# Performance work log

Hardware: AMD Instinct MI355X
Metric: run time of the kernel (lower is better)

## Reference

```python
import jax, jax.numpy as jnp
import numpy as np

NEG = -1e9  # stands in for -inf in masked_fill; identical softmax output, grad-safe


def _sfu(inputs, fusion, Wr, Wg):
    # SFU: m = [x, f, x*f, x-f]; o = relu(m@Wr)*g + (1-g)*x, g = sigmoid(m@Wg)
    m = jnp.concatenate([inputs, fusion, inputs * fusion, inputs - fusion], axis=-1)
    x = jax.nn.relu(m @ Wr)
    g = jax.nn.sigmoid(m @ Wg)
    return x * g + (1.0 - g) * inputs


def _stage(U, V, cmask, qmask, E, B, p):
    # One Aligner stage = InterAlign followed by SelfAlign. Batch-first layout (b, len, d).
    Wu, bu, Wv, bv, Wri, Wgi, gi, W1, b1, W2, b2, Wrs, Wgs, gs = p
    # ---- InterAlign ----
    Ct = jax.nn.relu(U @ Wu + bu)              # (b, c, d)
    Qt = jax.nn.relu(V @ Wv + bv)              # (b, q, d)
    E0 = jnp.einsum('bcd,bqd->bcq', Ct, Qt)    # (b, c, q)
    if E is not None:
        Es = jax.nn.softmax(jnp.where(cmask[:, :, None] == 0, NEG, E), axis=1)   # softmax over c
        Bs = jax.nn.softmax(jnp.where(cmask[:, None, :] == 0, NEG, B), axis=2)   # softmax over c (cols)
        E = E0 + gi * jnp.einsum('bce,beq->bcq', Bs, Es)
    else:
        E = E0
    Ett = jax.nn.softmax(jnp.where(qmask[:, None, :] == 0, NEG, E), axis=2)
    qctx = jnp.einsum('bcq,bqd->bcd', Ett, V)  # attend question
    h = _sfu(U, qctx, Wri, Wgi)
    # ---- SelfAlign ----
    H1 = jax.nn.relu(h @ W1 + b1)
    H2 = jax.nn.relu(h @ W2 + b2)
    B0 = jnp.einsum('bcd,bed->bce', H1, H2)    # (b, c, c)
    if B is not None:
        B1s = jax.nn.softmax(jnp.where(cmask[:, :, None] == 0, NEG, B), axis=1)
        B2s = jax.nn.softmax(jnp.where(cmask[:, None, :] == 0, NEG, B), axis=2)
        B = B0 + gs * jnp.einsum('bce,bef->bcf', B2s, B1s)
    else:
        B = B0
    c = U.shape[1]
    B = B * (1.0 - jnp.eye(c, dtype=B.dtype))[None]  # masked_fill_(eye, 0.0): zero diagonal
    Btt = jax.nn.softmax(jnp.where(cmask[:, None, :] == 0, NEG, B), axis=2)
    hctx = jnp.einsum('bce,bed->bcd', Btt, h)
    Z = _sfu(h, hctx, Wrs, Wgs)
    return Z, E, B


def setup_inputs() -> dict:
    key = jax.random.key(0)
    b, c_len, q_len, d = 8, 768, 96, 768
    T = 2  # number of aligner stages
    ks = jax.random.split(key, 16)
    s = 0.02
    inp = {
        'U': jax.random.normal(ks[0], (b, c_len, d), jnp.float32),
        'V': jax.random.normal(ks[1], (b, q_len, d), jnp.float32),
        'U_mask': jax.random.randint(ks[2], (b, c_len), 0, 2).astype(jnp.int32),
        'V_mask': jax.random.randint(ks[3], (b, q_len), 0, 2).astype(jnp.int32),
        'Wu': jax.random.normal(ks[4], (T, d, d), jnp.float32) * s,
        'bu': jnp.zeros((T, d), jnp.float32),
        'Wv': jax.random.normal(ks[5], (T, d, d), jnp.float32) * s,
        'bv': jnp.zeros((T, d), jnp.float32),
        'Wr_i': jax.random.normal(ks[6], (T, 4 * d, d), jnp.float32) * s,
        'Wg_i': jax.random.normal(ks[7], (T, 4 * d, d), jnp.float32) * s,
        'gamma_i': jnp.full((T,), 3.0, jnp.float32),
        'W1': jax.random.normal(ks[8], (T, d, d), jnp.float32) * s,
        'b1': jnp.zeros((T, d), jnp.float32),
        'W2': jax.random.normal(ks[9], (T, d, d), jnp.float32) * s,
        'b2': jnp.zeros((T, d), jnp.float32),
        'Wr_s': jax.random.normal(ks[10], (T, 4 * d, d), jnp.float32) * s,
        'Wg_s': jax.random.normal(ks[11], (T, 4 * d, d), jnp.float32) * s,
        'gamma_s': jnp.full((T,), 3.0, jnp.float32),
    }
    return inp


def reference(U, V, U_mask, V_mask, Wu, bu, Wv, bv, Wr_i, Wg_i, gamma_i,
              W1, b1, W2, b2, Wr_s, Wg_s, gamma_s):
    E = None
    B = None
    x = U
    for t in range(Wu.shape[0]):  # fixed small stage loop (align_1 -> align_2)
        p = (Wu[t], bu[t], Wv[t], bv[t], Wr_i[t], Wg_i[t], gamma_i[t],
             W1[t], b1[t], W2[t], b2[t], Wr_s[t], Wg_s[t], gamma_s[t])
        x, E, B = _stage(x, V, U_mask, V_mask, E, B, p)
    return x
```

## Files before the change

kernel.cpp:

```cpp
#include <hip/hip_runtime.h>
#include <math.h>

#define NEGV -1e9f

typedef short bf16x8 __attribute__((ext_vector_type(8)));
typedef float f32x4 __attribute__((ext_vector_type(4)));
typedef unsigned short ushort8v __attribute__((ext_vector_type(8)));

static __device__ __forceinline__ unsigned short f2bf(float f) {
  unsigned int u = __float_as_uint(f);
  unsigned int r = (u + 0x7fffu + ((u >> 16) & 1u)) >> 16;
  return (unsigned short)r;
}

static __device__ __forceinline__ int xcd_swz(int lin, int nwg) {
  int q = nwg >> 3, r = nwg & 7;
  int x = lin & 7, i = lin >> 3;
  return (x < r) ? x * (q + 1) + i : r * (q + 1) + (x - r) * q + i;
}

__device__ __forceinline__ float wred_max(float v) {
  #pragma unroll
  for (int o = 32; o > 0; o >>= 1) v = fmaxf(v, __shfl_down(v, o, 64));
  return v;
}
__device__ __forceinline__ float wred_sum(float v) {
  #pragma unroll
  for (int o = 32; o > 0; o >>= 1) v += __shfl_down(v, o, 64);
  return v;
}

__global__ __launch_bounds__(256)
void softmax_row_mask(const float* __restrict__ X, const int* __restrict__ mask,
                      float* __restrict__ Y, unsigned short* __restrict__ Ybf,
                      int R, int Cn)
{
  int bz = blockIdx.y, r = blockIdx.x, tid = threadIdx.x;
  const float* xr = X + ((size_t)bz * R + r) * Cn;
  const int*   mr = mask + (size_t)bz * Cn;
  float*       yr = Y ? (Y + ((size_t)bz * R + r) * Cn) : nullptr;
  unsigned short* yb = Ybf ? (Ybf + ((size_t)bz * R + r) * Cn) : nullptr;
  __shared__ float sred[4];

  float mx = -INFINITY;
  for (int i = tid; i < Cn; i += 256) {
    float v = (mr[i] != 0) ? xr[i] : NEGV;
    mx = fmaxf(mx, v);
  }
  float wm = wred_max(mx);
  if ((tid & 63) == 0) sred[tid >> 6] = wm;
  __syncthreads();
  mx = fmaxf(fmaxf(sred[0], sred[1]), fmaxf(sred[2], sred[3]));
  __syncthreads();

  float s = 0.f;
  for (int i = tid; i < Cn; i += 256) {
    float v = (mr[i] != 0) ? xr[i] : NEGV;
    s += expf(v - mx);
  }
  float wsv = wred_sum(s);
  if ((tid & 63) == 0) sred[tid >> 6] = wsv;
  __syncthreads();
  s = sred[0] + sred[1] + sred[2] + sred[3];
  float inv = 1.0f / s;

  for (int i = tid; i < Cn; i += 256) {
    float v = (mr[i] != 0) ? xr[i] : NEGV;
    float o = expf(v - mx) * inv;
    if (yr) yr[i] = o;
    if (yb) yb[i] = f2bf(o);
  }
}

__global__ __launch_bounds__(256)
void colsm_stats(const float* __restrict__ X, const int* __restrict__ mask,
                 float* __restrict__ SM, float* __restrict__ SS, int n)
{
  int bz = blockIdx.z;
  const float* Xb = X + (size_t)bz * n * n;
  const int*   mr = mask + (size_t)bz * n;
  __shared__ float T[64][65];
  __shared__ float rm[4][64], rs[4][64];
  int j0 = blockIdx.x * 64, i0 = blockIdx.y * 64;
  int t = threadIdx.x;
  int tr = t >> 4, tc4 = (t & 15) * 4;
  int jj = t & 63, qq = t >> 6;

  #pragma unroll
  for (int r = 0; r < 4; ++r) {
    int i = tr + r * 16;
    float4 v = *reinterpret_cast<const float4*>(Xb + (size_t)(i0 + i) * n + j0 + tc4);
    int mk = mr[i0 + i];
    T[i][tc4 + 0] = mk ? v.x : NEGV;
    T[i][tc4 + 1] = mk ? v.y : NEGV;
    T[i][tc4 + 2] = mk ? v.z : NEGV;
    T[i][tc4 + 3] = mk ? v.w : NEGV;
  }
  __syncthreads();
  float m = -INFINITY, s = 0.f;
  #pragma unroll
  for (int r = 0; r < 16; ++r) {
    float v = T[qq * 16 + r][jj];
    float nm = fmaxf(m, v);
    s = s * expf(m - nm) + expf(v - nm);
    m = nm;
  }
  rm[qq][jj] = m; rs[qq][jj] = s;
  __syncthreads();
  if (t < 64) {
    float m0 = rm[0][t], m1 = rm[1][t], m2 = rm[2][t], m3 = rm[3][t];
    float fm = fmaxf(fmaxf(m0, m1), fmaxf(m2, m3));
    float fs = rs[0][t] * expf(m0 - fm) + rs[1][t] * expf(m1 - fm)
             + rs[2][t] * expf(m2 - fm) + rs[3][t] * expf(m3 - fm);
    size_t base = (((size_t)bz * gridDim.x + blockIdx.x) * gridDim.y + blockIdx.y) * 64 + t;
    SM[base] = fm; SS[base] = fs;
  }
}

__global__ __launch_bounds__(256)
void colsm_emit(const float* __restrict__ X, const int* __restrict__ mask,
                const float* __restrict__ SM, const float* __restrict__ SS,
                unsigned short* __restrict__ Y, int n)
{
  int bz = blockIdx.z;
  const float* Xb = X + (size_t)bz * n * n;
  const int*   mr = mask + (size_t)bz * n;
  unsigned short* Yb = Y + (size_t)bz * n * n;
  __shared__ float T[64][65];
  __shared__ float sm[64], sinv[64];
  int j0 = blockIdx.x * 64, i0 = blockIdx.y * 64;
  int t = threadIdx.x;
  int tr = t >> 4, tc4 = (t & 15) * 4;
  int nt = gridDim.y;

  if (t < 64) {
    size_t base = (((size_t)bz * gridDim.x + blockIdx.x) * nt) * 64 + t;
    float fm = -INFINITY;
    for (int it = 0; it < nt; ++it) fm = fmaxf(fm, SM[base + (size_t)it * 64]);
    float fs = 0.f;
    for (int it = 0; it < nt; ++it)
      fs += SS[base + (size_t)it * 64] * expf(SM[base + (size_t)it * 64] - fm);
    sm[t] = fm; sinv[t] = 1.0f / fs;
  }
  #pragma unroll
  for (int r = 0; r < 4; ++r) {
    int i = tr + r * 16;
    float4 v = *reinterpret_cast<const float4*>(Xb + (size_t)(i0 + i) * n + j0 + tc4);
    int mk = mr[i0 + i];
    T[i][tc4 + 0] = mk ? v.x : NEGV;
    T[i][tc4 + 1] = mk ? v.y : NEGV;
    T[i][tc4 + 2] = mk ? v.z : NEGV;
    T[i][tc4 + 3] = mk ? v.w : NEGV;
  }
  __syncthreads();
  #pragma unroll
  for (int r = 0; r < 4; ++r) {
    int jr = tr + r * 16;
    float fm = sm[jr], inv = sinv[jr];
    ushort4 o;
    o.x = f2bf(expf(T[tc4 + 0][jr] - fm) * inv);
    o.y = f2bf(expf(T[tc4 + 1][jr] - fm) * inv);
    o.z = f2bf(expf(T[tc4 + 2][jr] - fm) * inv);
    o.w = f2bf(expf(T[tc4 + 3][jr] - fm) * inv);
    *reinterpret_cast<ushort4*>(Yb + (size_t)(j0 + jr) * n + i0 + tc4) = o;
  }
}

__global__ __launch_bounds__(256)
void transp_f32(const float* __restrict__ X, float* __restrict__ Y,
                int R, int C, long sX, long sY)
{
  int bz = blockIdx.z;
  X += (size_t)bz * sX;
  Y += (size_t)bz * sY;
  __shared__ float T[64][65];
  int c0 = blockIdx.x * 64, r0 = blockIdx.y * 64;
  int t = threadIdx.x;
  int tr = t >> 4, tc4 = (t & 15) * 4;
  #pragma unroll
  for (int rr = 0; rr < 4; ++rr) {
    int r = tr + rr * 16;
    float4 v = make_float4(0.f, 0.f, 0.f, 0.f);
    if (c0 + tc4 < C)
      v = *reinterpret_cast<const float4*>(X + (size_t)(r0 + r) * C + c0 + tc4);
    T[r][tc4 + 0] = v.x; T[r][tc4 + 1] = v.y;
    T[r][tc4 + 2] = v.z; T[r][tc4 + 3] = v.w;
  }
  __syncthreads();
  #pragma unroll
  for (int rr = 0; rr < 4; ++rr) {
    int cc = tr + rr * 16;
    int gc = c0 + cc;
    if (gc < C) {
      float4 o = make_float4(T[tc4 + 0][cc], T[tc4 + 1][cc], T[tc4 + 2][cc], T[tc4 + 3][cc]);
      *reinterpret_cast<float4*>(Y + (size_t)gc * R + r0 + tc4) = o;
    }
  }
}

__global__ __launch_bounds__(256)
void transpV(const float* __restrict__ V, unsigned short* __restrict__ VT)
{
  int bz = blockIdx.z;
  const float* Vb = V + (size_t)bz * 96 * 768;
  unsigned short* Yb = VT + (size_t)bz * 768 * 96;
  __shared__ float T[64][65];
  int c0 = blockIdx.x * 64, r0 = blockIdx.y * 64;
  int t = threadIdx.x;
  int tr = t >> 4, tc4 = (t & 15) * 4;
  #pragma unroll
  for (int rr = 0; rr < 4; ++rr) {
    int r = tr + rr * 16;
    int gr = r0 + r;
    float4 v = make_float4(0.f, 0.f, 0.f, 0.f);
    if (gr < 96)
      v = *reinterpret_cast<const float4*>(Vb + (size_t)gr * 768 + c0 + tc4);
    T[r][tc4 + 0] = v.x; T[r][tc4 + 1] = v.y;
    T[r][tc4 + 2] = v.z; T[r][tc4 + 3] = v.w;
  }
  __syncthreads();
  #pragma unroll
  for (int rr = 0; rr < 4; ++rr) {
    int cc = tr + rr * 16;
    int gc = c0 + cc;
    #pragma unroll
    for (int e = 0; e < 4; ++e) {
      int gr = r0 + tc4 + e;
      if (gr < 96) Yb[(size_t)gc * 96 + gr] = f2bf(T[tc4 + e][cc]);
    }
  }
}

__global__ __launch_bounds__(256)
void transp_cast4(const float* __restrict__ W0, const float* __restrict__ W1a,
                  const float* __restrict__ W2a, const float* __restrict__ W3a,
                  unsigned short* __restrict__ Wt)
{
  int z = blockIdx.z;
  const float* W = (z == 0) ? W0 : (z == 1) ? W1a : (z == 2) ? W2a : W3a;
  unsigned short* Y = Wt + (size_t)z * 768 * 768;
  __shared__ float T[64][65];
  int n0 = blockIdx.x * 64, k0 = blockIdx.y * 64;
  int t = threadIdx.x;
  int tr = t >> 4, tc4 = (t & 15) * 4;
  #pragma unroll
  for (int r = 0; r < 4; ++r) {
    int k = tr + r * 16;
    float4 v = *reinterpret_cast<const float4*>(W + (size_t)(k0 + k) * 768 + n0 + tc4);
    T[k][tc4 + 0] = v.x; T[k][tc4 + 1] = v.y; T[k][tc4 + 2] = v.z; T[k][tc4 + 3] = v.w;
  }
  __syncthreads();
  #pragma unroll
  for (int r = 0; r < 4; ++r) {
    int n = tr + r * 16;
    ushort4 o;
    o.x = f2bf(T[tc4 + 0][n]); o.y = f2bf(T[tc4 + 1][n]);
    o.z = f2bf(T[tc4 + 2][n]); o.w = f2bf(T[tc4 + 3][n]);
    *reinterpret_cast<ushort4*>(Y + (size_t)(n0 + n) * 768 + k0 + tc4) = o;
  }
}

__global__ __launch_bounds__(256)
void transp_cast2(const float* __restrict__ Wa, const float* __restrict__ Wb,
                  unsigned short* __restrict__ Wt)
{
  const float* W = blockIdx.z ? Wb : Wa;
  unsigned short* Y = Wt + (size_t)blockIdx.z * 768 * 2304;
  __shared__ float T[64][65];
  int n0 = blockIdx.x * 64, k0 = blockIdx.y * 64;
  int t = threadIdx.x;
  int tr = t >> 4, tc4 = (t & 15) * 4;
  #pragma unroll
  for (int r = 0; r < 4; ++r) {
    int k = tr + r * 16;
    int gk = k0 + k;
    float4 v = *reinterpret_cast<const float4*>(W + (size_t)gk * 768 + n0 + tc4);
    if (gk < 768) {
      float4 u = *reinterpret_cast<const float4*>(W + (size_t)(gk + 2304) * 768 + n0 + tc4);
      v.x += u.x; v.y += u.y; v.z += u.z; v.w += u.w;
    } else if (gk < 1536) {
      float4 u = *reinterpret_cast<const float4*>(W + (size_t)(gk + 1536) * 768 + n0 + tc4);
      v.x -= u.x; v.y -= u.y; v.z -= u.z; v.w -= u.w;
    }
    T[k][tc4 + 0] = v.x; T[k][tc4 + 1] = v.y; T[k][tc4 + 2] = v.z; T[k][tc4 + 3] = v.w;
  }
  __syncthreads();
  #pragma unroll
  for (int r = 0; r < 4; ++r) {
    int n = tr + r * 16;
    ushort4 o;
    o.x = f2bf(T[tc4 + 0][n]); o.y = f2bf(T[tc4 + 1][n]);
    o.z = f2bf(T[tc4 + 2][n]); o.w = f2bf(T[tc4 + 3][n]);
    *reinterpret_cast<ushort4*>(Y + (size_t)(n0 + n) * 2304 + k0 + tc4) = o;
  }
}

__global__ __launch_bounds__(256)
void transp_cast(const float* __restrict__ W, unsigned short* __restrict__ Wt,
                 int K, long sW, long sWt)
{
  int bz = blockIdx.z;
  W  += (size_t)bz * sW;
  Wt += (size_t)bz * sWt;
  __shared__ float T[64][65];
  int n0 = blockIdx.x * 64, k0 = blockIdx.y * 64;
  int t = threadIdx.x;
  int tr = t >> 4, tc4 = (t & 15) * 4;
  #pragma unroll
  for (int r = 0; r < 4; ++r) {
    int k = tr + r * 16;
    float4 v = *reinterpret_cast<const float4*>(W + (size_t)(k0 + k) * 768 + n0 + tc4);
    T[k][tc4 + 0] = v.x; T[k][tc4 + 1] = v.y; T[k][tc4 + 2] = v.z; T[k][tc4 + 3] = v.w;
  }
  __syncthreads();
  #pragma unroll
  for (int r = 0; r < 4; ++r) {
    int n = tr + r * 16;
    ushort4 o;
    o.x = f2bf(T[tc4 + 0][n]); o.y = f2bf(T[tc4 + 1][n]);
    o.z = f2bf(T[tc4 + 2][n]); o.w = f2bf(T[tc4 + 3][n]);
    *reinterpret_cast<ushort4*>(Wt + (size_t)(n0 + n) * K + k0 + tc4) = o;
  }
}

__global__ __launch_bounds__(256)
void cast_bf16(const float* __restrict__ X, unsigned short* __restrict__ Y, int n8)
{
  int idx = blockIdx.x * 256 + threadIdx.x;
  if (idx >= n8) return;
  float4 a0 = *reinterpret_cast<const float4*>(X + (size_t)idx * 8);
  float4 a1 = *reinterpret_cast<const float4*>(X + (size_t)idx * 8 + 4);
  ushort8v o;
  o[0] = f2bf(a0.x); o[1] = f2bf(a0.y); o[2] = f2bf(a0.z); o[3] = f2bf(a0.w);
  o[4] = f2bf(a1.x); o[5] = f2bf(a1.y); o[6] = f2bf(a1.z); o[7] = f2bf(a1.w);
  *reinterpret_cast<ushort8v*>(Y + (size_t)idx * 8) = o;
}


template<int NB, int WAVES>
__global__ __launch_bounds__(64 * WAVES)
void mfma_gemm(const unsigned short* __restrict__ A,
               const unsigned short* __restrict__ Bt0,
               const unsigned short* __restrict__ Bt1,
               const float* __restrict__ bias0, const float* __restrict__ bias1,
               const float* __restrict__ alphap, const float* __restrict__ C0,
               float* __restrict__ F0, float* __restrict__ F1,
               unsigned short* __restrict__ O0, unsigned short* __restrict__ O1,
               int M, int N, int K,
               long sA, long sB, long sC0, long sC,
               int relu, int zerodiag,
               const float* __restrict__ Xc, unsigned short* __restrict__ McO)
{
  const int RG = WAVES / 4;
  const int TM = RG * 48;
  __shared__ unsigned short As[2][TM * 32];
  __shared__ unsigned short Bs0[2][2048];
  __shared__ unsigned short Bs1[2][NB == 2 ? 2048 : 16];

  int nx = gridDim.x, ny = gridDim.y;
  int nwg = nx * ny * gridDim.z;
  int lin = blockIdx.x + nx * (blockIdx.y + ny * blockIdx.z);
  int sw = xcd_swz(lin, nwg);
  int bxi = sw % nx; int rest = sw / nx;
  int byi = rest % ny; int bz = rest / ny;

  A   += (size_t)bz * sA;
  Bt0 += (size_t)bz * sB;
  if (NB == 2) Bt1 += (size_t)bz * sB;
  const float* C0b = C0 ? (C0 + (size_t)bz * sC0) : nullptr;

  int tid = threadIdx.x;
  int w = tid >> 6, l = tid & 63;
  int m0 = byi * TM, n0 = bxi * 64;
  int wr = w >> 2, wc = w & 3;

  int g8 = (((l & 3) ^ ((l >> 3) & 3))) * 8;
  int rowA = w * 16 + (l >> 2); if (rowA > TM - 1) rowA = TM - 1;
  int rB = n0 + (w & 3) * 16 + (l >> 2); if (rB > N - 1) rB = N - 1;
  const unsigned short* srcA  = A + (size_t)(m0 + rowA) * K + g8;
  const unsigned short* srcB0 = Bt0 + (size_t)rB * K + g8;
  const unsigned short* srcB1 = (NB == 2) ? Bt1 + (size_t)rB * K + g8 : nullptr;

#define GG_STAGE(kt, bi) do { int kk0 = (kt) * 32;                                                                        \
    if (w < TM / 16)                                                                                                      \
      __builtin_amdgcn_global_load_lds((const unsigned int*)(srcA + kk0),  (unsigned int*)&As[bi][0]  + w * 256, 16, 0, 0); \
    if (w < 4)                                                                                                            \
      __builtin_amdgcn_global_load_lds((const unsigned int*)(srcB0 + kk0), (unsigned int*)&Bs0[bi][0] + w * 256, 16, 0, 0); \
    if (NB == 2 && w >= 4)                                                                                                \
      __builtin_amdgcn_global_load_lds((const unsigned int*)(srcB1 + kk0), (unsigned int*)&Bs1[bi][0] + (w - 4) * 256, 16, 0, 0); \
  } while (0)

  f32x4 a0[3] = {};
  f32x4 a1v[3] = {};

  const int NT = K / 32;
  int prm = ((l >> 4) ^ ((l >> 1) & 3)) * 8;
  GG_STAGE(0, 0);
  __syncthreads();
  int cur = 0;
  for (int kt = 0; kt < NT; ++kt) {
    if (kt + 1 < NT) GG_STAGE(kt + 1, cur ^ 1);

    bf16x8 af[3];
    #pragma unroll
    for (int i = 0; i < 3; ++i) {
      int off = (wr * 48 + i * 16 + (l & 15)) * 32 + prm;
      af[i] = *reinterpret_cast<const bf16x8*>(&As[cur][off]);
    }
    int offB = (wc * 16 + (l & 15)) * 32 + prm;
    bf16x8 b0 = *reinterpret_cast<const bf16x8*>(&Bs0[cur][offB]);
    #pragma unroll
    for (int i = 0; i < 3; ++i)
      a0[i] = __builtin_amdgcn_mfma_f32_16x16x32_bf16(af[i], b0, a0[i], 0, 0, 0);
    if (NB == 2) {
      bf16x8 b1 = *reinterpret_cast<const bf16x8*>(&Bs1[cur][offB]);
      #pragma unroll
      for (int i = 0; i < 3; ++i)
        a1v[i] = __builtin_amdgcn_mfma_f32_16x16x32_bf16(af[i], b1, a1v[i], 0, 0, 0);
    }
    __syncthreads();
    cur ^= 1;
  }
#undef GG_STAGE

  float alpha = alphap ? alphap[0] : 1.0f;
  float* F0b = F0 ? F0 + (size_t)bz * sC : nullptr;
  float* F1b = F1 ? F1 + (size_t)bz * sC : nullptr;
  unsigned short* O0b = O0 ? O0 + (size_t)bz * sC : nullptr;
  unsigned short* O1b = O1 ? O1 + (size_t)bz * sC : nullptr;
  const float* Xcb = Xc ? Xc + (size_t)bz * 589824 : nullptr;
  unsigned short* Mcb = McO ? McO + (size_t)bz * 1769472 : nullptr;

  #pragma unroll
  for (int i = 0; i < 3; ++i) {
    #pragma unroll
    for (int qq = 0; qq < 4; ++qq) {
      int gm = m0 + wr * 48 + i * 16 + (l >> 4) * 4 + qq;
      int gn = n0 + wc * 16 + (l & 15);
      if (gn >= N) continue;
      size_t oidx = (size_t)gm * N + gn;
      float v = alpha * a0[i][qq];
      if (bias0) v += bias0[gn];
      if (relu) v = fmaxf(v, 0.f);
      if (C0b) v += C0b[oidx];
      if (zerodiag && gm == gn) v = 0.f;
      if (Mcb) {
        float xv = Xcb[(size_t)gm * 768 + gn];
        size_t mrow = (size_t)gm * 2304 + gn;
        Mcb[mrow]        = f2bf(xv);
        Mcb[mrow + 768]  = f2bf(v);
        Mcb[mrow + 1536] = f2bf(xv * v);
      }
      if (F0b) F0b[oidx] = v;
      if (O0b) O0b[oidx] = f2bf(v);
      if (NB == 2) {
        float v1 = alpha * a1v[i][qq];
        if (bias1) v1 += bias1[gn];
        if (relu) v1 = fmaxf(v1, 0.f);
        if (F1b) F1b[oidx] = v1;
        if (O1b) O1b[oidx] = f2bf(v1);
      }
    }
  }
}

__global__ __launch_bounds__(512)
void mfma_dual2(const unsigned short* __restrict__ A1,
                const unsigned short* __restrict__ B1t,
                const unsigned short* __restrict__ A2,
                const unsigned short* __restrict__ B2t,
                const float* __restrict__ alphap, float* __restrict__ F0,
                int M, int N, int K,
                long sA1, long sB1, long sA2, long sB2, long sC,
                int zerodiag)
{
  __shared__ unsigned short As1[2][3072], Bs1[2][2048];
  __shared__ unsigned short As2[2][3072], Bs2[2][2048];

  int nx = gridDim.x, ny = gridDim.y;
  int nwg = nx * ny * gridDim.z;
  int lin = blockIdx.x + nx * (blockIdx.y + ny * blockIdx.z);
  int sw = xcd_swz(lin, nwg);
  int bxi = sw % nx; int rest = sw / nx;
  int byi = rest % ny; int bz = rest / ny;

  A1  += (size_t)bz * sA1;
  B1t += (size_t)bz * sB1;
  A2  += (size_t)bz * sA2;
  B2t += (size_t)bz * sB2;

  int tid = threadIdx.x;
  int w = tid >> 6, l = tid & 63;
  int m0 = byi * 96, n0 = bxi * 64;
  int wr = w >> 2, wc = w & 3;

  int g8 = (((l & 3) ^ ((l >> 3) & 3))) * 8;
  int rowA = w * 16 + (l >> 2); if (rowA > 95) rowA = 95;
  int rB = n0 + (w & 3) * 16 + (l >> 2);
  const unsigned short* srcA1 = A1 + (size_t)(m0 + rowA) * K + g8;
  const unsigned short* srcA2 = A2 + (size_t)(m0 + rowA) * K + g8;
  const unsigned short* srcB1 = B1t + (size_t)rB * K + g8;
  const unsigned short* srcB2 = B2t + (size_t)rB * K + g8;

#define D2_STAGE(kt, bi) do { int kk0 = (kt) * 32;                                                                        \
    if (w < 6) {                                                                                                          \
      __builtin_amdgcn_global_load_lds((const unsigned int*)(srcA1 + kk0), (unsigned int*)&As1[bi][0] + w * 256, 16, 0, 0); \
      __builtin_amdgcn_global_load_lds((const unsigned int*)(srcA2 + kk0), (unsigned int*)&As2[bi][0] + w * 256, 16, 0, 0); \
    }                                                                                                                     \
    if (w < 4)                                                                                                            \
      __builtin_amdgcn_global_load_lds((const unsigned int*)(srcB1 + kk0), (unsigned int*)&Bs1[bi][0] + w * 256, 16, 0, 0); \
    else                                                                                                                  \
      __builtin_amdgcn_global_load_lds((const unsigned int*)(srcB2 + kk0), (unsigned int*)&Bs2[bi][0] + (w - 4) * 256, 16, 0, 0); \
  } while (0)

  f32x4 ac1[3] = {};
  f32x4 ac2[3] = {};

  const int NT = K / 32;
  int prm = ((l >> 4) ^ ((l >> 1) & 3)) * 8;
  D2_STAGE(0, 0);
  __syncthreads();
  int cur = 0;
  for (int kt = 0; kt < NT; ++kt) {
    if (kt + 1 < NT) D2_STAGE(kt + 1, cur ^ 1);

    int offB = (wc * 16 + (l & 15)) * 32 + prm;
    bf16x8 af1[3], af2[3];
    #pragma unroll
    for (int i = 0; i < 3; ++i) {
      int off = (wr * 48 + i * 16 + (l & 15)) * 32 + prm;
      af1[i] = *reinterpret_cast<const bf16x8*>(&As1[cur][off]);
      af2[i] = *reinterpret_cast<const bf16x8*>(&As2[cur][off]);
    }
    bf16x8 b1 = *reinterpret_cast<const bf16x8*>(&Bs1[cur][offB]);
    bf16x8 b2 = *reinterpret_cast<const bf16x8*>(&Bs2[cur][offB]);
    #pragma unroll
    for (int i = 0; i < 3; ++i) {
      ac1[i] = __builtin_amdgcn_mfma_f32_16x16x32_bf16(af1[i], b1, ac1[i], 0, 0, 0);
      ac2[i] = __builtin_amdgcn_mfma_f32_16x16x32_bf16(af2[i], b2, ac2[i], 0, 0, 0);
    }
    __syncthreads();
    cur ^= 1;
  }
#undef D2_STAGE

  float alpha = alphap[0];
  float* F0b = F0 + (size_t)bz * sC;
  #pragma unroll
  for (int i = 0; i < 3; ++i) {
    #pragma unroll
    for (int qq = 0; qq < 4; ++qq) {
      int gm = m0 + wr * 48 + i * 16 + (l >> 4) * 4 + qq;
      int gn = n0 + wc * 16 + (l & 15);
      float v = ac1[i][qq] + alpha * ac2[i][qq];
      if (zerodiag && gm == gn) v = 0.f;
      F0b[(size_t)gm * N + gn] = v;
    }
  }
}

__global__ __launch_bounds__(512)
void sfu_mfma(const unsigned short* __restrict__ Mc,
              const unsigned short* __restrict__ Brt,
              const unsigned short* __restrict__ Bgt,
              const float* __restrict__ Xres, float* __restrict__ Z,
              unsigned short* __restrict__ Zb)
{
  __shared__ unsigned short As[2][3072];
  __shared__ unsigned short Brs[2][2048];
  __shared__ unsigned short Bgs[2][2048];
  const int K = 2304;
  const int NT = 72;

  int nx = gridDim.x, ny = gridDim.y;
  int nwg = nx * ny;
  int lin = blockIdx.x + nx * blockIdx.y;
  int sw = xcd_swz(lin, nwg);
  int bxi = sw % nx; int byi = sw / nx;

  int tid = threadIdx.x;
  int w = tid >> 6, l = tid & 63;
  int m0 = byi * 96, n0 = bxi * 64;
  int wr = w >> 2, wc = w & 3;

  int g8 = (((l & 3) ^ ((l >> 3) & 3))) * 8;
  int rowA = w * 16 + (l >> 2); if (rowA > 95) rowA = 95;
  int rB = n0 + (w & 3) * 16 + (l >> 2);
  const unsigned short* srcA = Mc  + (size_t)(m0 + rowA) * K + g8;
  const unsigned short* srcR = Brt + (size_t)rB * K + g8;
  const unsigned short* srcG = Bgt + (size_t)rB * K + g8;

#define SFU_STAGE(kt, bi) do { int kk0 = (kt) * 32;                                                                      \
    if (w < 6)                                                                                                           \
      __builtin_amdgcn_global_load_lds((const unsigned int*)(srcA + kk0), (unsigned int*)&As[bi][0]  + w * 256, 16, 0, 0); \
    if (w < 4)                                                                                                           \
      __builtin_amdgcn_global_load_lds((const unsigned int*)(srcR + kk0), (unsigned int*)&Brs[bi][0] + w * 256, 16, 0, 0); \
    if (w >= 4)                                                                                                          \
      __builtin_amdgcn_global_load_lds((const unsigned int*)(srcG + kk0), (unsigned int*)&Bgs[bi][0] + (w - 4) * 256, 16, 0, 0); \
  } while (0)

  f32x4 aR[3] = {};
  f32x4 aG[3] = {};

  int prm = ((l >> 4) ^ ((l >> 1) & 3)) * 8;
  SFU_STAGE(0, 0);
  __syncthreads();
  int cur = 0;
  for (int kt = 0; kt < NT; ++kt) {
    if (kt + 1 < NT) SFU_STAGE(kt + 1, cur ^ 1);

    bf16x8 af[3];
    #pragma unroll
    for (int i = 0; i < 3; ++i) {
      int off = (wr * 48 + i * 16 + (l & 15)) * 32 + prm;
      af[i] = *reinterpret_cast<const bf16x8*>(&As[cur][off]);
    }
    int offB = (wc * 16 + (l & 15)) * 32 + prm;
    bf16x8 br = *reinterpret_cast<const bf16x8*>(&Brs[cur][offB]);
    bf16x8 bg = *reinterpret_cast<const bf16x8*>(&Bgs[cur][offB]);
    #pragma unroll
    for (int i = 0; i < 3; ++i) {
      aR[i] = __builtin_amdgcn_mfma_f32_16x16x32_bf16(af[i], br, aR[i], 0, 0, 0);
      aG[i] = __builtin_amdgcn_mfma_f32_16x16x32_bf16(af[i], bg, aG[i], 0, 0, 0);
    }
    __syncthreads();
    cur ^= 1;
  }
#undef SFU_STAGE

  #pragma unroll
  for (int i = 0; i < 3; ++i) {
    #pragma unroll
    for (int qq = 0; qq < 4; ++qq) {
      int gm = m0 + wr * 48 + i * 16 + (l >> 4) * 4 + qq;
      int gn = n0 + wc * 16 + (l & 15);
      float r = fmaxf(aR[i][qq], 0.f);
      float g = 1.0f / (1.0f + expf(-aG[i][qq]));
      float xv = Xres[(size_t)gm * 768 + gn];
      float z = r * g + (1.0f - g) * xv;
      Z[(size_t)gm * 768 + gn] = z;
      if (Zb) Zb[(size_t)gm * 768 + gn] = f2bf(z);
    }
  }
}

static void launch_mfma1(const unsigned short* A, const unsigned short* Bt,
                         const float* bias, const float* alphap, const float* C0,
                         float* F0, unsigned short* O0,
                         int M, int N, int K, long sA, long sB, long sC0, long sC,
                         int relu, int zd, int batch, int tm, hipStream_t s,
                         const float* xcat = nullptr, unsigned short* mco = nullptr)
{
  dim3 g((N + 63) / 64, M / tm, batch);
  if (tm == 48)
    mfma_gemm<1, 4><<<g, 256, 0, s>>>(A, Bt, nullptr, bias, nullptr, alphap, C0,
                                      F0, nullptr, O0, nullptr, M, N, K, sA, sB, sC0, sC, relu, zd,
                                      xcat, mco);
  else
    mfma_gemm<1, 8><<<g, 512, 0, s>>>(A, Bt, nullptr, bias, nullptr, alphap, C0,
                                      F0, nullptr, O0, nullptr, M, N, K, sA, sB, sC0, sC, relu, zd,
                                      xcat, mco);
}

static void launch_mfma2(const unsigned short* A, const unsigned short* Bt0,
                         const unsigned short* Bt1, const float* bias0, const float* bias1,
                         unsigned short* O0, unsigned short* O1,
                         int M, int N, int K, long sA, long sB,
                         int relu, int batch, hipStream_t s)
{
  dim3 g((N + 63) / 64, M / 96, batch);
  mfma_gemm<2, 8><<<g, 512, 0, s>>>(A, Bt0, Bt1, bias0, bias1, nullptr, nullptr,
                                    nullptr, nullptr, O0, O1, M, N, K, sA, sB, 0, sA,
                                    relu, 0, nullptr, nullptr);
}

static void launch_sfu_tail(const float* Wr, const float* Wg, const float* xres,
                            float* z, unsigned short* zb,
                            unsigned short* Mc, unsigned short* Wt, hipStream_t s)
{
  unsigned short* Wrt = Wt;
  unsigned short* Wgt = Wt + (size_t)768 * 2304;
  transp_cast2<<<dim3(12, 36, 2), 256, 0, s>>>(Wr, Wg, Wt);
  sfu_mfma<<<dim3(12, 64), 512, 0, s>>>(Mc, Wrt, Wgt, xres, z, zb);
}

extern "C" void kernel_launch(void* const* d_in, const int* in_sizes, int n_in,
                              void* d_out, int out_size, void* d_ws, size_t ws_size,
                              hipStream_t stream)
{
  const int b = 8, c = 768, q = 96, d = 768, T = 2;
  const float* U   = (const float*)d_in[0];
  const float* V   = (const float*)d_in[1];
  const int*   Um  = (const int*)d_in[2];
  const int*   Vm  = (const int*)d_in[3];
  const float* Wu  = (const float*)d_in[4];
  const float* bu  = (const float*)d_in[5];
  const float* Wv  = (const float*)d_in[6];
  const float* bv  = (const float*)d_in[7];
  const float* Wri = (const float*)d_in[8];
  const float* Wgi = (const float*)d_in[9];
  const float* gi  = (const float*)d_in[10];
  const float* W1  = (const float*)d_in[11];
  const float* b1  = (const float*)d_in[12];
  const float* W2  = (const float*)d_in[13];
  const float* b2  = (const float*)d_in[14];
  const float* Wrs = (const float*)d_in[15];
  const float* Wgs = (const float*)d_in[16];
  const float* gs  = (const float*)d_in[17];
  float* out = (float*)d_out;

  const size_t big = (size_t)b * c * d;
  const size_t smE = (size_t)b * c * q;
  float* ws   = (float*)d_ws;
  float* xbuf = ws + 0 * big;
  float* h    = ws + 1 * big;
  float* Bm   = ws + 2 * big;
  float* t1   = ws + 3 * big;
  float* t2   = ws + 4 * big;
  float* t3   = ws + 5 * big;
  float* t4   = ws + 6 * big;
  float* Ebuf = ws + 7 * big;
  float* E0b  = Ebuf + smE;
  float* Esb  = E0b + smE;
  float* spare = Esb + smE;
  float* slotE = spare + smE;
  float* WTf  = slotE + big / 2;

  unsigned short* Mc  = (unsigned short*)t1;
  unsigned short* Wt  = (unsigned short*)t4;
  unsigned short* t1h = (unsigned short*)t1;
  unsigned short* t3h = (unsigned short*)t3;
  unsigned short* t3h2 = t3h + big;
  unsigned short* slotEb = (unsigned short*)slotE;
  unsigned short* H1b = t1h;
  unsigned short* H2b = H1b + big;
  float* SMst = spare;
  float* SSst = spare + 73728;
  unsigned short* WuT = (unsigned short*)WTf;
  unsigned short* WvT  = WuT  + (size_t)d * d;
  unsigned short* W1T  = WvT  + (size_t)d * d;
  unsigned short* W2T  = W1T  + (size_t)d * d;
  unsigned short* Vb16 = W2T  + (size_t)d * d;
  unsigned short* Qtbb = Vb16 + smE;
  unsigned short* VTb  = Qtbb + smE;
  unsigned short* EsTb = VTb  + smE;
  unsigned short* Ettb = EsTb + smE;

  const long cd = (long)c * d, cq = (long)c * q, qd = (long)q * d, cc = (long)c * c;
  const size_t dd = (size_t)d * d;
  const int cast_big = (int)(big / 8);
  (void)ws_size;

  const float* x = U;
  for (int t = 0; t < T; ++t) {
    const float* Writ = Wri + (size_t)t * 4 * dd;
    const float* Wgit = Wgi + (size_t)t * 4 * dd;
    const float* Wrst = Wrs + (size_t)t * 4 * dd;
    const float* Wgst = Wgs + (size_t)t * 4 * dd;

    transp_cast4<<<dim3(12, 12, 4), 256, 0, stream>>>(Wu + t * dd, Wv + t * dd,
                                                      W1 + t * dd, W2 + t * dd, WuT);
    if (t == 0) {
      cast_bf16<<<dim3((int)(smE / 8 / 256)), 256, 0, stream>>>(V, Vb16, (int)(smE / 8));
      transpV<<<dim3(12, 2, b), 256, 0, stream>>>(V, VTb);
      cast_bf16<<<dim3(cast_big / 256), 256, 0, stream>>>(x, t3h, cast_big);
    }

    launch_mfma1(t3h, WuT, bu + t * d, nullptr, nullptr, nullptr, t1h,
                 b * c, d, d, 0, 0, 0, 0, 1, 0, 1, 96, stream);
    launch_mfma1(Vb16, WvT, bv + t * d, nullptr, nullptr, nullptr, Qtbb,
                 b * q, d, d, 0, 0, 0, 0, 1, 0, 1, 48, stream);
    float* e0dst = (t == 0) ? Ebuf : E0b;
    launch_mfma1(t1h, Qtbb, nullptr, nullptr, nullptr, e0dst, nullptr,
                 c, q, d, cd, qd, 0, cq, 0, 0, b, 48, stream);
    if (t > 0) {
      transp_f32<<<dim3(2, 12, b), 256, 0, stream>>>(Ebuf, Esb, c, q, cq, cq);
      softmax_row_mask<<<dim3(q, b), 256, 0, stream>>>(Esb, Um, nullptr, EsTb, q, c);
      softmax_row_mask<<<dim3(c, b), 256, 0, stream>>>(Bm, Um, nullptr, slotEb, c, c);
      launch_mfma1(slotEb, EsTb, nullptr, gi + t, E0b, Ebuf, nullptr,
                   c, q, c, cc, cq, cq, cq, 0, 0, b, 48, stream);
    }
    softmax_row_mask<<<dim3(c, b), 256, 0, stream>>>(Ebuf, Vm, nullptr, Ettb, c, q);
    launch_mfma1(Ettb, VTb, nullptr, nullptr, nullptr, nullptr, nullptr,
                 c, d, q, cq, qd, 0, cd, 0, 0, b, 96, stream, x, Mc);
    launch_sfu_tail(Writ, Wgit, x, h, t3h, Mc, Wt, stream);
    launch_mfma2(t3h, W1T, W2T, b1 + t * d, b2 + t * d, H1b, H2b,
                 b * c, d, d, 0, 0, 1, 1, stream);
    if (t == 0) {
      launch_mfma1(H1b, H2b, nullptr, nullptr, nullptr, Bm, nullptr,
                   c, c, d, cd, cd, 0, cc, 0, 1, b, 96, stream);
    } else {
      colsm_stats<<<dim3(12, 12, b), 256, 0, stream>>>(Bm, Um, SMst, SSst, c);
      colsm_emit<<<dim3(12, 12, b), 256, 0, stream>>>(Bm, Um, SMst, SSst, t3h2, c);
      mfma_dual2<<<dim3(12, 8, b), 512, 0, stream>>>(H1b, H2b, slotEb, t3h2,
                                                     gs + t, Bm,
                                                     c, c, d, cd, cd, cc, cc, cc, 1);
    }
    softmax_row_mask<<<dim3(c, b), 256, 0, stream>>>(Bm, Um, nullptr, t3h2, c, c);
    transp_cast<<<dim3(12, 12, b), 256, 0, stream>>>(h, slotEb, 768, cd, cd);
    launch_mfma1(t3h2, slotEb, nullptr, nullptr, nullptr, nullptr, nullptr,
                 c, d, c, cc, cd, 0, cd, 0, 0, b, 96, stream, h, Mc);
    float* zdst = (t == T - 1) ? out : xbuf;
    unsigned short* zb16 = (t == T - 1) ? nullptr : t3h;
    launch_sfu_tail(Wrst, Wgst, h, zdst, zb16, Mc, Wt, stream);

    x = xbuf;
  }
}
```

Baseline: 714.1 us.

## Fuse Ct/Qt projections, fuse question softmax into qctx GEMM, transpose bf16 h

Result: faster. 669.3 us (-6.3%).

```diff
diff --git a/kernel.cpp b/kernel.cpp
--- a/kernel.cpp
+++ b/kernel.cpp
@@ -199,6 +199,34 @@
 }
 
 __global__ __launch_bounds__(256)
+void transp_bf16(const unsigned short* __restrict__ X, unsigned short* __restrict__ Y)
+{
+  int bz = blockIdx.z;
+  X += (size_t)bz * 589824;
+  Y += (size_t)bz * 589824;
+  __shared__ unsigned short T[64][65];
+  int c0 = blockIdx.x * 64, r0 = blockIdx.y * 64;
+  int t = threadIdx.x;
+  int tr = t >> 4, tc4 = (t & 15) * 4;
+  #pragma unroll
+  for (int rr = 0; rr < 4; ++rr) {
+    int r = tr + rr * 16;
+    ushort4 v = *reinterpret_cast<const ushort4*>(X + (size_t)(r0 + r) * 768 + c0 + tc4);
+    T[r][tc4 + 0] = v.x; T[r][tc4 + 1] = v.y;
+    T[r][tc4 + 2] = v.z; T[r][tc4 + 3] = v.w;
+  }
+  __syncthreads();
+  #pragma unroll
+  for (int rr = 0; rr < 4; ++rr) {
+    int cc = tr + rr * 16;
+    ushort4 o;
+    o.x = T[tc4 + 0][cc]; o.y = T[tc4 + 1][cc];
+    o.z = T[tc4 + 2][cc]; o.w = T[tc4 + 3][cc];
+    *reinterpret_cast<ushort4*>(Y + (size_t)(c0 + cc) * 768 + r0 + tc4) = o;
+  }
+}
+
+__global__ __launch_bounds__(256)
 void transpV(const float* __restrict__ V, unsigned short* __restrict__ VT)
 {
   int bz = blockIdx.z;
@@ -292,34 +320,6 @@
     o.x = f2bf(T[tc4 + 0][n]); o.y = f2bf(T[tc4 + 1][n]);
     o.z = f2bf(T[tc4 + 2][n]); o.w = f2bf(T[tc4 + 3][n]);
     *reinterpret_cast<ushort4*>(Y + (size_t)(n0 + n) * 2304 + k0 + tc4) = o;
-  }
-}
-
-__global__ __launch_bounds__(256)
-void transp_cast(const float* __restrict__ W, unsigned short* __restrict__ Wt,
-                 int K, long sW, long sWt)
-{
-  int bz = blockIdx.z;
-  W  += (size_t)bz * sW;
-  Wt += (size_t)bz * sWt;
-  __shared__ float T[64][65];
-  int n0 = blockIdx.x * 64, k0 = blockIdx.y * 64;
-  int t = threadIdx.x;
-  int tr = t >> 4, tc4 = (t & 15) * 4;
-  #pragma unroll
-  for (int r = 0; r < 4; ++r) {
-    int k = tr + r * 16;
-    float4 v = *reinterpret_cast<const float4*>(W + (size_t)(k0 + k) * 768 + n0 + tc4);
-    T[k][tc4 + 0] = v.x; T[k][tc4 + 1] = v.y; T[k][tc4 + 2] = v.z; T[k][tc4 + 3] = v.w;
-  }
-  __syncthreads();
-  #pragma unroll
-  for (int r = 0; r < 4; ++r) {
-    int n = tr + r * 16;
-    ushort4 o;
-    o.x = f2bf(T[tc4 + 0][n]); o.y = f2bf(T[tc4 + 1][n]);
-    o.z = f2bf(T[tc4 + 2][n]); o.w = f2bf(T[tc4 + 3][n]);
-    *reinterpret_cast<ushort4*>(Wt + (size_t)(n0 + n) * K + k0 + tc4) = o;
   }
 }
 
@@ -465,6 +465,190 @@
 }
 
 __global__ __launch_bounds__(512)
+void mfma_relu_pair(const unsigned short* __restrict__ A1g,
+                    const unsigned short* __restrict__ B1g,
+                    const float* __restrict__ bias1g, unsigned short* __restrict__ O1g,
+                    const unsigned short* __restrict__ A2g,
+                    const unsigned short* __restrict__ B2g,
+                    const float* __restrict__ bias2g, unsigned short* __restrict__ O2g)
+{
+  const int K = 768, N = 768, NT = 24;
+  __shared__ unsigned short As[2][3072];
+  __shared__ unsigned short Bs0[2][2048];
+
+  int nx = gridDim.x, ny = gridDim.y;
+  int nwg = nx * ny;
+  int lin = blockIdx.x + nx * blockIdx.y;
+  int sw = xcd_swz(lin, nwg);
+  int bxi = sw % nx; int byi = sw / nx;
+
+  const unsigned short* A; const unsigned short* Bt;
+  const float* bias; unsigned short* O;
+  int m0;
+  if (byi < 64) { A = A1g; Bt = B1g; bias = bias1g; O = O1g; m0 = byi * 96; }
+  else          { A = A2g; Bt = B2g; bias = bias2g; O = O2g; m0 = (byi - 64) * 96; }
+
+  int tid = threadIdx.x;
+  int w = tid >> 6, l = tid & 63;
+  int n0 = bxi * 64;
+  int wr = w >> 2, wc = w & 3;
+
+  int g8 = (((l & 3) ^ ((l >> 3) & 3))) * 8;
+  int rowA = w * 16 + (l >> 2); if (rowA > 95) rowA = 95;
+  int rB = n0 + (w & 3) * 16 + (l >> 2);
+  const unsigned short* srcA  = A + (size_t)(m0 + rowA) * K + g8;
+  const unsigned short* srcB0 = Bt + (size_t)rB * K + g8;
+
+#define RP_STAGE(kt, bi) do { int kk0 = (kt) * 32;                                                                        \
+    if (w < 6)                                                                                                            \
+      __builtin_amdgcn_global_load_lds((const unsigned int*)(srcA + kk0),  (unsigned int*)&As[bi][0]  + w * 256, 16, 0, 0); \
+    if (w < 4)                                                                                                            \
+      __builtin_amdgcn_global_load_lds((const unsigned int*)(srcB0 + kk0), (unsigned int*)&Bs0[bi][0] + w * 256, 16, 0, 0); \
+  } while (0)
+
+  f32x4 a0[3] = {};
+  int prm = ((l >> 4) ^ ((l >> 1) & 3)) * 8;
+  RP_STAGE(0, 0);
+  __syncthreads();
+  int cur = 0;
+  for (int kt = 0; kt < NT; ++kt) {
+    if (kt + 1 < NT) RP_STAGE(kt + 1, cur ^ 1);
+
+    bf16x8 af[3];
+    #pragma unroll
+    for (int i = 0; i < 3; ++i) {
+      int off = (wr * 48 + i * 16 + (l & 15)) * 32 + prm;
+      af[i] = *reinterpret_cast<const bf16x8*>(&As[cur][off]);
+    }
+    int offB = (wc * 16 + (l & 15)) * 32 + prm;
+    bf16x8 b0 = *reinterpret_cast<const bf16x8*>(&Bs0[cur][offB]);
+    #pragma unroll
+    for (int i = 0; i < 3; ++i)
+      a0[i] = __builtin_amdgcn_mfma_f32_16x16x32_bf16(af[i], b0, a0[i], 0, 0, 0);
+    __syncthreads();
+    cur ^= 1;
+  }
+#undef RP_STAGE
+
+  #pragma unroll
+  for (int i = 0; i < 3; ++i) {
+    #pragma unroll
+    for (int qq = 0; qq < 4; ++qq) {
+      int gm = m0 + wr * 48 + i * 16 + (l >> 4) * 4 + qq;
+      int gn = n0 + wc * 16 + (l & 15);
+      float v = a0[i][qq] + bias[gn];
+      v = fmaxf(v, 0.f);
+      O[(size_t)gm * N + gn] = f2bf(v);
+    }
+  }
+}
+
+__global__ __launch_bounds__(512)
+void qctx_fused(const float* __restrict__ E, const int* __restrict__ Vm,
+                const unsigned short* __restrict__ VTb,
+                const float* __restrict__ X, unsigned short* __restrict__ Mc)
+{
+  __shared__ unsigned short As3[3][3072];
+  __shared__ unsigned short Bs3[3][2048];
+  __shared__ int mk[96];
+
+  int nx = gridDim.x, ny = gridDim.y;
+  int nwg = nx * ny * gridDim.z;
+  int lin = blockIdx.x + nx * (blockIdx.y + ny * blockIdx.z);
+  int sw = xcd_swz(lin, nwg);
+  int bxi = sw % nx; int rest = sw / nx;
+  int byi = rest % ny; int bz = rest / ny;
+
+  int tid = threadIdx.x;
+  int w = tid >> 6, l = tid & 63;
+  int m0 = byi * 96, n0 = bxi * 64;
+
+  int g8 = (((l & 3) ^ ((l >> 3) & 3))) * 8;
+  if (w < 4) {
+    int rB = n0 + w * 16 + (l >> 2);
+    const unsigned short* srcB = VTb + ((size_t)bz * 768 + rB) * 96 + g8;
+    #pragma unroll
+    for (int kt = 0; kt < 3; ++kt)
+      __builtin_amdgcn_global_load_lds((const unsigned int*)(srcB + kt * 32),
+                                       (unsigned int*)&Bs3[kt][0] + w * 256, 16, 0, 0);
+  }
+  if (tid < 96) mk[tid] = Vm[bz * 96 + tid];
+  __syncthreads();
+
+  if (tid < 384) {
+    int r = tid >> 2, j4 = tid & 3;
+    const float* er = E + ((size_t)bz * 768 + m0 + r) * 96 + j4 * 24;
+    float va[24];
+    #pragma unroll
+    for (int u = 0; u < 6; ++u) {
+      float4 v = *reinterpret_cast<const float4*>(er + u * 4);
+      int kb = j4 * 24 + u * 4;
+      va[u * 4 + 0] = mk[kb + 0] ? v.x : NEGV;
+      va[u * 4 + 1] = mk[kb + 1] ? v.y : NEGV;
+      va[u * 4 + 2] = mk[kb + 2] ? v.z : NEGV;
+      va[u * 4 + 3] = mk[kb + 3] ? v.w : NEGV;
+    }
+    float mx = -INFINITY;
+    #pragma unroll
+    for (int u = 0; u < 24; ++u) mx = fmaxf(mx, va[u]);
+    mx = fmaxf(mx, __shfl_xor(mx, 1, 64));
+    mx = fmaxf(mx, __shfl_xor(mx, 2, 64));
+    float s = 0.f;
+    #pragma unroll
+    for (int u = 0; u < 24; ++u) { va[u] = expf(va[u] - mx); s += va[u]; }
+    s += __shfl_xor(s, 1, 64);
+    s += __shfl_xor(s, 2, 64);
+    float inv = 1.0f / s;
+    #pragma unroll
+    for (int g = 0; g < 3; ++g) {
+      int gG = j4 * 3 + g;
+      int kt = gG >> 2, Gin = gG & 3;
+      ushort8v o;
+      #pragma unroll
+      for (int e = 0; e < 8; ++e) o[e] = f2bf(va[g * 8 + e] * inv);
+      int idx = (r >> 4) * 512 + ((r & 15) * 4 + (Gin ^ ((r >> 1) & 3))) * 8;
+      *reinterpret_cast<ushort8v*>(&As3[kt][idx]) = o;
+    }
+  }
+  __syncthreads();
+
+  int wr = w >> 2, wc = w & 3;
+  int prm = ((l >> 4) ^ ((l >> 1) & 3)) * 8;
+  f32x4 acc[3] = {};
+  #pragma unroll
+  for (int kt = 0; kt < 3; ++kt) {
+    bf16x8 af[3];
+    #pragma unroll
+    for (int i = 0; i < 3; ++i) {
+      int off = (wr * 48 + i * 16 + (l & 15)) * 32 + prm;
+      af[i] = *reinterpret_cast<const bf16x8*>(&As3[kt][off]);
+    }
+    int offB = (wc * 16 + (l & 15)) * 32 + prm;
+    bf16x8 b0 = *reinterpret_cast<const bf16x8*>(&Bs3[kt][offB]);
+    #pragma unroll
+    for (int i = 0; i < 3; ++i)
+      acc[i] = __builtin_amdgcn_mfma_f32_16x16x32_bf16(af[i], b0, acc[i], 0, 0, 0);
+  }
+
+  const float* Xb = X + (size_t)bz * 589824;
+  unsigned short* Mcb = Mc + (size_t)bz * 1769472;
+  #pragma unroll
+  for (int i = 0; i < 3; ++i) {
+    #pragma unroll
+    for (int qq = 0; qq < 4; ++qq) {
+      int gm = m0 + wr * 48 + i * 16 + (l >> 4) * 4 + qq;
+      int gn = n0 + wc * 16 + (l & 15);
+      float v = acc[i][qq];
+      float xv = Xb[(size_t)gm * 768 + gn];
+      size_t mrow = (size_t)gm * 2304 + gn;
+      Mcb[mrow]        = f2bf(xv);
+      Mcb[mrow + 768]  = f2bf(v);
+      Mcb[mrow + 1536] = f2bf(xv * v);
+    }
+  }
+}
+
+__global__ __launch_bounds__(512)
 void mfma_dual2(const unsigned short* __restrict__ A1,
                 const unsigned short* __restrict__ B1t,
                 const unsigned short* __restrict__ A2,
@@ -749,7 +933,7 @@
   const long cd = (long)c * d, cq = (long)c * q, qd = (long)q * d, cc = (long)c * c;
   const size_t dd = (size_t)d * d;
   const int cast_big = (int)(big / 8);
-  (void)ws_size;
+  (void)ws_size; (void)Ettb;
 
   const float* x = U;
   for (int t = 0; t < T; ++t) {
@@ -766,10 +950,8 @@
       cast_bf16<<<dim3(cast_big / 256), 256, 0, stream>>>(x, t3h, cast_big);
     }
 
-    launch_mfma1(t3h, WuT, bu + t * d, nullptr, nullptr, nullptr, t1h,
-                 b * c, d, d, 0, 0, 0, 0, 1, 0, 1, 96, stream);
-    launch_mfma1(Vb16, WvT, bv + t * d, nullptr, nullptr, nullptr, Qtbb,
-                 b * q, d, d, 0, 0, 0, 0, 1, 0, 1, 48, stream);
+    mfma_relu_pair<<<dim3(12, 72), 512, 0, stream>>>(t3h, WuT, bu + t * d, t1h,
+                                                     Vb16, WvT, bv + t * d, Qtbb);
     float* e0dst = (t == 0) ? Ebuf : E0b;
     launch_mfma1(t1h, Qtbb, nullptr, nullptr, nullptr, e0dst, nullptr,
                  c, q, d, cd, qd, 0, cq, 0, 0, b, 48, stream);
@@ -780,9 +962,7 @@
       launch_mfma1(slotEb, EsTb, nullptr, gi + t, E0b, Ebuf, nullptr,
                    c, q, c, cc, cq, cq, cq, 0, 0, b, 48, stream);
     }
-    softmax_row_mask<<<dim3(c, b), 256, 0, stream>>>(Ebuf, Vm, nullptr, Ettb, c, q);
-    launch_mfma1(Ettb, VTb, nullptr, nullptr, nullptr, nullptr, nullptr,
-                 c, d, q, cq, qd, 0, cd, 0, 0, b, 96, stream, x, Mc);
+    qctx_fused<<<dim3(12, 8, b), 512, 0, stream>>>(Ebuf, Vm, VTb, x, Mc);
     launch_sfu_tail(Writ, Wgit, x, h, t3h, Mc, Wt, stream);
     launch_mfma2(t3h, W1T, W2T, b1 + t * d, b2 + t * d, H1b, H2b,
                  b * c, d, d, 0, 0, 1, 1, stream);
@@ -797,7 +977,7 @@
                                                      c, c, d, cd, cd, cc, cc, cc, 1);
     }
     softmax_row_mask<<<dim3(c, b), 256, 0, stream>>>(Bm, Um, nullptr, t3h2, c, c);
-    transp_cast<<<dim3(12, 12, b), 256, 0, stream>>>(h, slotEb, 768, cd, cd);
+    transp_bf16<<<dim3(12, 12, b), 256, 0, stream>>>(t3h, slotEb);
     launch_mfma1(t3h2, slotEb, nullptr, nullptr, nullptr, nullptr, nullptr,
                  c, d, c, cc, cd, 0, cd, 0, 0, b, 96, stream, h, Mc);
     float* zdst = (t == T - 1) ? out : xbuf;
```
